# Optimization experiments

Measured on AMD Instinct MI355X. Metric: run time of the kernel, lower is better.

Reference implementation:

```python
import jax, jax.numpy as jnp
import numpy as np

D = 1024
H = 16
HD = D // H
FF = 4 * D
LN_EPS = 1e-5


def _layernorm(x, w, b):
    mu = jnp.mean(x, axis=-1, keepdims=True)
    var = jnp.mean(jnp.square(x - mu), axis=-1, keepdims=True)
    return (x - mu) * jax.lax.rsqrt(var + LN_EPS) * w + b


def setup_inputs() -> dict:
    key = jax.random.key(0)
    ks = jax.random.split(key, 12)
    s = 0.02
    return {
        "x": jax.random.normal(ks[0], (8, 1024, D), jnp.float32),
        "c": jax.random.normal(ks[1], (8, D), jnp.float32),
        "ln1_w": jnp.ones((D,), jnp.float32),
        "ln1_b": jnp.zeros((D,), jnp.float32),
        "ln2_w": jnp.ones((D,), jnp.float32),
        "ln2_b": jnp.zeros((D,), jnp.float32),
        "ada_w": jax.random.normal(ks[2], (D, 6 * D), jnp.float32) * s,
        "ada_b": jnp.zeros((6 * D,), jnp.float32),
        "qkv_w": jax.random.normal(ks[3], (D, 3 * D), jnp.float32) * s,
        "qkv_b": jnp.zeros((3 * D,), jnp.float32),
        "proj_w": jax.random.normal(ks[4], (D, D), jnp.float32) * s,
        "proj_b": jnp.zeros((D,), jnp.float32),
        "fc1_w": jax.random.normal(ks[5], (D, FF), jnp.float32) * s,
        "fc1_b": jnp.zeros((FF,), jnp.float32),
        "fc2_w": jax.random.normal(ks[6], (FF, D), jnp.float32) * s,
        "fc2_b": jnp.zeros((D,), jnp.float32),
    }


def reference(x, c, ln1_w, ln1_b, ln2_w, ln2_b, ada_w, ada_b,
              qkv_w, qkv_b, proj_w, proj_b, fc1_w, fc1_b, fc2_w, fc2_b):
    B, L, _ = x.shape
    # adaLN modulation: SiLU(c) @ W -> 6 chunks of (B, D)
    ssg = jax.nn.silu(c) @ ada_w + ada_b
    msa_shift, msa_scale, msa_gate, mlp_shift, mlp_scale, mlp_gate = jnp.split(ssg, 6, axis=-1)

    def modulate(h, shift, scale):
        return h * (1.0 + scale[:, None, :]) + shift[:, None, :]

    # ---- attention branch ----
    h = modulate(_layernorm(x, ln1_w, ln1_b), msa_shift, msa_scale)
    qkv = h @ qkv_w + qkv_b                      # (B, L, 3D)
    q, k, v = jnp.split(qkv, 3, axis=-1)
    q = q.reshape(B, L, H, HD).transpose(0, 2, 1, 3)   # (B, H, L, HD)
    k = k.reshape(B, L, H, HD).transpose(0, 2, 1, 3)
    v = v.reshape(B, L, H, HD).transpose(0, 2, 1, 3)
    scores = jnp.einsum("bhqd,bhkd->bhqk", q, k) / jnp.sqrt(jnp.float32(HD))
    attn = jax.nn.softmax(scores, axis=-1)
    a = jnp.einsum("bhqk,bhkd->bhqd", attn, v)   # (B, H, L, HD)
    a = a.transpose(0, 2, 1, 3).reshape(B, L, D)
    a = a @ proj_w + proj_b
    x = x + msa_gate[:, None, :] * a

    # ---- MLP branch ----
    h = modulate(_layernorm(x, ln2_w, ln2_b), mlp_shift, mlp_scale)
    h = jax.nn.gelu(h @ fc1_w + fc1_b, approximate=True)
    h = h @ fc2_w + fc2_b
    x = x + mlp_gate[:, None, :] * h
    return x
```

## Files before the change

### kernel.cpp

```cpp
#include <hip/hip_runtime.h>
#include <math.h>

#define DMODEL 1024
#define SIXD   6144
#define NHEAD  16
#define HEADD  64
#define LSEQ   1024
#define NBATCH 8
#define MROWS  8192

typedef unsigned short ushort_t;
typedef __attribute__((ext_vector_type(8))) short bf16x8;
typedef __attribute__((ext_vector_type(4))) float f32x4;

__device__ __forceinline__ unsigned short f2bf(float f) {
  unsigned int u = __float_as_uint(f);
  u += 0x7fff + ((u >> 16) & 1);
  return (unsigned short)(u >> 16);
}

__device__ __forceinline__ void gload_lds16(const void* g, void* l) {
  __builtin_amdgcn_global_load_lds(
      (const __attribute__((address_space(1))) unsigned int*)g,
      (__attribute__((address_space(3))) unsigned int*)l, 16, 0, 0);
}

__global__ void tcast_kernel(const float* __restrict__ W, ushort_t* __restrict__ WT,
                             int K, int N) {
  __shared__ float tile[32][33];
  int tx = threadIdx.x & 31, ty = threadIdx.x >> 5;
  int n0 = blockIdx.x * 32, k0 = blockIdx.y * 32;
#pragma unroll
  for (int r = 0; r < 4; ++r)
    tile[ty + 8*r][tx] = W[(size_t)(k0 + ty + 8*r) * N + n0 + tx];
  __syncthreads();
#pragma unroll
  for (int r = 0; r < 4; ++r)
    WT[(size_t)(n0 + ty + 8*r) * K + k0 + tx] = f2bf(tile[tx][ty + 8*r]);
}

__global__ __launch_bounds__(256) void vtrans_kernel(
    const ushort_t* __restrict__ qkvb, ushort_t* __restrict__ vT) {
  __shared__ ushort_t tile[128][66];
  int bh = blockIdx.x;
  int kt = blockIdx.y;
  int b = bh >> 4, h = bh & 15;
  int tid = threadIdx.x;
#pragma unroll
  for (int i = 0; i < 4; ++i) {
    int flat = tid + 256 * i;
    int r = flat >> 3, c8 = flat & 7;
    bf16x8 v = *(const bf16x8*)((const short*)qkvb +
        (size_t)(b * LSEQ + kt * 128 + r) * 3072 + 2048 + h * 64 + c8 * 8);
#pragma unroll
    for (int j = 0; j < 8; ++j) tile[r][c8 * 8 + j] = (ushort_t)v[j];
  }
  __syncthreads();
#pragma unroll
  for (int i = 0; i < 4; ++i) {
    int d = i * 16 + (tid >> 4);
    int kc = tid & 15;
    bf16x8 ov;
#pragma unroll
    for (int j = 0; j < 8; ++j) ov[j] = (short)tile[kc * 8 + j][d];
    *(bf16x8*)((short*)vT + (size_t)(bh * 64 + d) * 1024 + kt * 128 + kc * 8) = ov;
  }
}

__global__ void ada_kernel(const float* __restrict__ c, const float* __restrict__ ada_w,
                           const float* __restrict__ ada_b, float* __restrict__ ssg) {
  __shared__ float s[DMODEL];
  int b = blockIdx.y;
  int j = blockIdx.x * 256 + threadIdx.x;
  for (int i = threadIdx.x; i < DMODEL; i += 256) {
    float v = c[b * DMODEL + i];
    s[i] = v / (1.0f + __expf(-v));
  }
  __syncthreads();
  float acc = ada_b[j];
#pragma unroll 8
  for (int k = 0; k < DMODEL; ++k)
    acc = fmaf(s[k], ada_w[(size_t)k * SIXD + j], acc);
  ssg[b * SIXD + j] = acc;
}

__global__ __launch_bounds__(256) void ln_mod_kernel(
    const float* __restrict__ xin, const float* __restrict__ lw,
    const float* __restrict__ lb, const float* __restrict__ ssg,
    int shift_off, int scale_off, ushort_t* __restrict__ outB) {
  int row = blockIdx.x;
  int b = row >> 10;
  int tid = threadIdx.x;
  float4 v = ((const float4*)xin)[(size_t)row * 256 + tid];
  float sum = v.x + v.y + v.z + v.w;
  float sq  = v.x*v.x + v.y*v.y + v.z*v.z + v.w*v.w;
#pragma unroll
  for (int m = 32; m; m >>= 1) { sum += __shfl_xor(sum, m); sq += __shfl_xor(sq, m); }
  __shared__ float rbuf[8];
  int w = tid >> 6, lane = tid & 63;
  if (lane == 0) { rbuf[w] = sum; rbuf[4 + w] = sq; }
  __syncthreads();
  sum = rbuf[0] + rbuf[1] + rbuf[2] + rbuf[3];
  sq  = rbuf[4] + rbuf[5] + rbuf[6] + rbuf[7];
  float mu  = sum * (1.0f / 1024.0f);
  float var = sq * (1.0f / 1024.0f) - mu * mu;
  float rs  = rsqrtf(var + 1e-5f);
  const float* sg = ssg + b * SIXD;
  float vv[4] = {v.x, v.y, v.z, v.w};
  ushort4 pk;
  unsigned short* pks = (unsigned short*)&pk;
#pragma unroll
  for (int j = 0; j < 4; ++j) {
    int d = tid * 4 + j;
    float h = (vv[j] - mu) * rs * lw[d] + lb[d];
    h = h * (1.0f + sg[scale_off + d]) + sg[shift_off + d];
    pks[j] = f2bf(h);
  }
  ((ushort4*)outB)[(size_t)row * 256 + tid] = pk;
}

template <int EPI>
__global__ __launch_bounds__(256, 2) void gemm_kernel(
    const ushort_t* __restrict__ A, const ushort_t* __restrict__ BT,
    const float* __restrict__ bias, const float* __restrict__ ssg,
    const float* resid, float* outF, ushort_t* __restrict__ outB,
    int N, int K, int gate_off) {
  __shared__ __align__(16) char As[16384];
  __shared__ __align__(16) char Bs[16384];
  int tid = threadIdx.x, lane = tid & 63, w = tid >> 6;
  int l15 = lane & 15, g = lane >> 4;
  int m0 = blockIdx.y * 128, n0 = blockIdx.x * 128;
  int wrow = (w >> 1) * 64, wcol = (w & 1) * 64;
  f32x4 zero = {0.f, 0.f, 0.f, 0.f};
  f32x4 acc[4][4];
#pragma unroll
  for (int i = 0; i < 4; ++i)
#pragma unroll
    for (int j = 0; j < 4; ++j) acc[i][j] = zero;

  for (int k0 = 0; k0 < K; k0 += 64) {
#pragma unroll
    for (int p = 0; p < 4; ++p) {
      int flat = p * 4096 + w * 1024 + lane * 16;
      int row = flat >> 7;
      int colb = (flat & 127) ^ ((row & 7) << 4);
      gload_lds16((const char*)A  + ((size_t)(m0 + row) * K + k0) * 2 + colb,
                  As + p * 4096 + w * 1024);
      gload_lds16((const char*)BT + ((size_t)(n0 + row) * K + k0) * 2 + colb,
                  Bs + p * 4096 + w * 1024);
    }
    __syncthreads();
#pragma unroll
    for (int kk = 0; kk < 2; ++kk) {
      bf16x8 af[4], bfr[4];
#pragma unroll
      for (int i = 0; i < 4; ++i) {
        int ar = wrow + i * 16 + l15;
        af[i]  = *(const bf16x8*)(As + ar * 128 + ((kk * 64 + g * 16) ^ ((ar & 7) << 4)));
        int br = wcol + i * 16 + l15;
        bfr[i] = *(const bf16x8*)(Bs + br * 128 + ((kk * 64 + g * 16) ^ ((br & 7) << 4)));
      }
#pragma unroll
      for (int i = 0; i < 4; ++i)
#pragma unroll
        for (int j = 0; j < 4; ++j)
          acc[i][j] = __builtin_amdgcn_mfma_f32_16x16x32_bf16(af[i], bfr[j], acc[i][j], 0, 0, 0);
    }
    __syncthreads();
  }
#pragma unroll
  for (int i = 0; i < 4; ++i)
#pragma unroll
    for (int j = 0; j < 4; ++j)
#pragma unroll
      for (int r = 0; r < 4; ++r) {
        int grow = m0 + wrow + i * 16 + g * 4 + r;
        int gcol = n0 + wcol + j * 16 + l15;
        float v = acc[i][j][r] + bias[gcol];
        if (EPI == 0) {
          outB[(size_t)grow * N + gcol] = f2bf(v);
        } else if (EPI == 1 || EPI == 3) {
          int bb = grow >> 10;
          float gate = ssg[bb * SIXD + gate_off + gcol];
          size_t idx = (size_t)grow * N + gcol;
          outF[idx] = resid[idx] + gate * v;
        } else {
          float u = v;
          float t = 0.7978845608028654f * (u + 0.044715f * u * u * u);
          float e = __expf(2.0f * t);
          float th = 1.0f - 2.0f / (e + 1.0f);
          outB[(size_t)grow * N + gcol] = f2bf(0.5f * u * (1.0f + th));
        }
      }
}

__global__ __launch_bounds__(256, 2) void attn_kernel(
    const ushort_t* __restrict__ qkv,
    const ushort_t* __restrict__ vT,
    ushort_t* __restrict__ aout) {
  __shared__ __align__(16) char SM[33024];
  float* alphab = (float*)(SM + 32768);
  int tid = threadIdx.x, lane = tid & 63, w = tid >> 6;
  int l15 = lane & 15, g = lane >> 4;
  int qt = blockIdx.x, bh = blockIdx.y;
  int b = bh >> 4, h = bh & 15;

  bf16x8 aq[2];
  {
    int qrow = qt * 64 + w * 16 + l15;
    const short* qp = (const short*)qkv + (size_t)(b * LSEQ + qrow) * 3072 + h * 64 + g * 8;
    aq[0] = *(const bf16x8*)qp;
    aq[1] = *(const bf16x8*)(qp + 32);
  }

  const char* ksrc[2];
  const char* vsrc[2];
#pragma unroll
  for (int p = 0; p < 2; ++p) {
    int flat = p * 4096 + w * 1024 + lane * 16;
    int row = flat >> 7;
    int colb = (flat & 127) ^ ((row & 7) << 4);
    ksrc[p] = (const char*)qkv + ((size_t)(b * LSEQ + row) * 3072 + 1024 + h * 64) * 2 + colb;
    vsrc[p] = (const char*)vT + ((size_t)(bh * 64 + row) * 1024) * 2 + colb;
  }

  f32x4 zero = {0.f, 0.f, 0.f, 0.f};
  f32x4 o[4] = {zero, zero, zero, zero};
  float mrow = -INFINITY;
  float lrow = 0.f;
  const float sc = 0.18033688f;

#pragma unroll
  for (int p = 0; p < 2; ++p) {
    gload_lds16(ksrc[p], SM + p * 4096 + w * 1024);
    gload_lds16(vsrc[p], SM + 16384 + p * 4096 + w * 1024);
  }
  __syncthreads();

  for (int t = 0; t < 16; ++t) {
    int cur = t & 1;
    if (t < 15) {
      size_t koff = (size_t)(t + 1) * (64 * 3072 * 2);
      size_t voff = (size_t)(t + 1) * 128;
#pragma unroll
      for (int p = 0; p < 2; ++p) {
        gload_lds16(ksrc[p] + koff, SM + (cur ^ 1) * 8192 + p * 4096 + w * 1024);
        gload_lds16(vsrc[p] + voff, SM + 16384 + (cur ^ 1) * 8192 + p * 4096 + w * 1024);
      }
    }
    f32x4 s4[4] = {zero, zero, zero, zero};
#pragma unroll
    for (int c = 0; c < 4; ++c)
#pragma unroll
      for (int ks = 0; ks < 2; ++ks) {
        int key = c * 16 + l15;
        bf16x8 ak = *(const bf16x8*)(SM + cur * 8192 + key * 128 +
                                     ((ks * 64 + g * 16) ^ ((key & 7) << 4)));
        s4[c] = __builtin_amdgcn_mfma_f32_16x16x32_bf16(ak, aq[ks], s4[c], 0, 0, 0);
      }
    float z[16], mx = -INFINITY;
#pragma unroll
    for (int c = 0; c < 4; ++c)
#pragma unroll
      for (int r = 0; r < 4; ++r) {
        float t2 = s4[c][r] * sc;
        z[c * 4 + r] = t2;
        mx = fmaxf(mx, t2);
      }
    mx = fmaxf(mx, __shfl_xor(mx, 16));
    mx = fmaxf(mx, __shfl_xor(mx, 32));
    bool need = __any(mx > mrow);
    if (need) {
      float mnew = fmaxf(mrow, mx);
      float alpha = exp2f(mrow - mnew);
      mrow = mnew;
      if (lane < 16) alphab[w * 16 + lane] = alpha;
      lrow *= alpha;
    }
    float p16[16], sump = 0.f;
#pragma unroll
    for (int i = 0; i < 16; ++i) {
      float p = exp2f(z[i] - mrow);
      p16[i] = p;
      sump += p;
    }
    sump += __shfl_xor(sump, 16);
    sump += __shfl_xor(sump, 32);
    lrow += sump;
    if (need) {
      f32x4 av = *(const f32x4*)&alphab[w * 16 + g * 4];
#pragma unroll
      for (int nb = 0; nb < 4; ++nb)
#pragma unroll
        for (int r = 0; r < 4; ++r) o[nb][r] *= av[r];
    }
    unsigned pk[8];
#pragma unroll
    for (int c = 0; c < 4; ++c)
#pragma unroll
      for (int m = 0; m < 2; ++m)
        asm("v_cvt_pk_bf16_f32 %0, %1, %2"
            : "=v"(pk[c * 2 + m]) : "v"(p16[c * 4 + 2 * m]), "v"(p16[c * 4 + 2 * m + 1]));
    unsigned pa[2][4];
    int gl = (g & 1) * 2;
#pragma unroll
    for (int kb = 0; kb < 2; ++kb)
#pragma unroll
      for (int wv = 0; wv < 4; ++wv) {
        int srcl = l15 + (gl + (wv >> 1)) * 16;
        unsigned vA = (unsigned)__shfl((int)pk[kb * 4 + (wv & 1)], srcl);
        unsigned vB = (unsigned)__shfl((int)pk[kb * 4 + 2 + (wv & 1)], srcl);
        pa[kb][wv] = (g >> 1) ? vB : vA;
      }
    union PU { unsigned u[4]; bf16x8 v; };
    PU pu0, pu1;
#pragma unroll
    for (int i = 0; i < 4; ++i) { pu0.u[i] = pa[0][i]; pu1.u[i] = pa[1][i]; }
#pragma unroll
    for (int kb = 0; kb < 2; ++kb)
#pragma unroll
      for (int nb = 0; nb < 4; ++nb) {
        int d = nb * 16 + l15;
        bf16x8 bv = *(const bf16x8*)(SM + 16384 + cur * 8192 + d * 128 +
                                     ((kb * 64 + g * 16) ^ ((d & 7) << 4)));
        o[nb] = __builtin_amdgcn_mfma_f32_16x16x32_bf16(kb ? pu1.v : pu0.v, bv, o[nb], 0, 0, 0);
      }
    __syncthreads();
  }
  if (lane < 16) alphab[w * 16 + lane] = 1.0f / lrow;
  f32x4 rl = *(const f32x4*)&alphab[w * 16 + g * 4];
#pragma unroll
  for (int nb = 0; nb < 4; ++nb)
#pragma unroll
    for (int r = 0; r < 4; ++r) {
      int qrow = qt * 64 + w * 16 + g * 4 + r;
      aout[(size_t)(b * LSEQ + qrow) * 1024 + h * 64 + nb * 16 + l15] =
          f2bf(o[nb][r] * rl[r]);
    }
}

extern "C" void kernel_launch(void* const* d_in, const int* in_sizes, int n_in,
                              void* d_out, int out_size, void* d_ws, size_t ws_size,
                              hipStream_t stream) {
  const float* x      = (const float*)d_in[0];
  const float* c      = (const float*)d_in[1];
  const float* ln1_w  = (const float*)d_in[2];
  const float* ln1_b  = (const float*)d_in[3];
  const float* ln2_w  = (const float*)d_in[4];
  const float* ln2_b  = (const float*)d_in[5];
  const float* ada_w  = (const float*)d_in[6];
  const float* ada_b  = (const float*)d_in[7];
  const float* qkv_w  = (const float*)d_in[8];
  const float* qkv_b  = (const float*)d_in[9];
  const float* proj_w = (const float*)d_in[10];
  const float* proj_b = (const float*)d_in[11];
  const float* fc1_w  = (const float*)d_in[12];
  const float* fc1_b  = (const float*)d_in[13];
  const float* fc2_w  = (const float*)d_in[14];
  const float* fc2_b  = (const float*)d_in[15];
  float* out = (float*)d_out;
  char* ws = (char*)d_ws;

  ushort_t* qkvT  = (ushort_t*)(ws + 0);
  ushort_t* projT = (ushort_t*)(ws + 6291456);
  ushort_t* fc1T  = (ushort_t*)(ws + 8388608);
  ushort_t* fc2T  = (ushort_t*)(ws + 16777216);
  float*    ssg   = (float*)(ws + 25165824);
  ushort_t* hbuf  = (ushort_t*)(ws + 25362432);
  ushort_t* abuf  = hbuf;
  ushort_t* qkvb  = (ushort_t*)(ws + 42139648);
  ushort_t* vTb   = (ushort_t*)(ws + 92471296);
  if (ws_size < (size_t)109248512) return;

  tcast_kernel<<<dim3(96, 32),  256, 0, stream>>>(qkv_w,  qkvT, 1024, 3072);
  tcast_kernel<<<dim3(32, 32),  256, 0, stream>>>(proj_w, projT, 1024, 1024);
  tcast_kernel<<<dim3(128, 32), 256, 0, stream>>>(fc1_w,  fc1T, 1024, 4096);
  tcast_kernel<<<dim3(32, 128), 256, 0, stream>>>(fc2_w,  fc2T, 4096, 1024);
  ada_kernel<<<dim3(24, 8), 256, 0, stream>>>(c, ada_w, ada_b, ssg);

  ln_mod_kernel<<<8192, 256, 0, stream>>>(x, ln1_w, ln1_b, ssg, 0, 1024, hbuf);
  gemm_kernel<0><<<dim3(24, 64), 256, 0, stream>>>(hbuf, qkvT, qkv_b, nullptr,
                                                   nullptr, nullptr, qkvb, 3072, 1024, 0);
  vtrans_kernel<<<dim3(128, 8), 256, 0, stream>>>(qkvb, vTb);
  attn_kernel<<<dim3(16, 128), 256, 0, stream>>>(qkvb, vTb, abuf);
  gemm_kernel<1><<<dim3(8, 64), 256, 0, stream>>>(abuf, projT, proj_b, ssg,
                                                  x, out, nullptr, 1024, 1024, 2048);
  ln_mod_kernel<<<8192, 256, 0, stream>>>(out, ln2_w, ln2_b, ssg, 3072, 4096, hbuf);
  gemm_kernel<2><<<dim3(32, 64), 256, 0, stream>>>(hbuf, fc1T, fc1_b, nullptr,
                                                   nullptr, nullptr, qkvb, 4096, 1024, 0);
  gemm_kernel<3><<<dim3(8, 64), 256, 0, stream>>>(qkvb, fc2T, fc2_b, ssg,
                                                  out, out, nullptr, 1024, 4096, 5120);
}
```

Measured before the change: 443.2 us.

## Restructure GEMM into 256x128 tiles with triple-buffered LDS pipeline and XCD swizzle

Rewrites the bf16 MFMA GEMM to use 512-thread blocks with 256x128 output tiles and a three-stage global-to-LDS pipeline using direct LDS loads. Explicit vmcnt waits and raw barriers overlap loads with compute, and s_setprio raises priority during the MFMA section. Block indices are remapped so neighbouring tiles land on the same XCD for L2 reuse. This trades 144KB of LDS per block, allowing only one block per CU, for less load latency exposure and better operand reuse.

```diff
diff --git a/kernel.cpp b/kernel.cpp
--- a/kernel.cpp
+++ b/kernel.cpp
@@ -120,74 +120,113 @@
 }
 
 template <int EPI>
-__global__ __launch_bounds__(256, 2) void gemm_kernel(
+__global__ __launch_bounds__(512, 2) void gemm_kernel(
     const ushort_t* __restrict__ A, const ushort_t* __restrict__ BT,
     const float* __restrict__ bias, const float* __restrict__ ssg,
     const float* resid, float* outF, ushort_t* __restrict__ outB,
-    int N, int K, int gate_off) {
-  __shared__ __align__(16) char As[16384];
-  __shared__ __align__(16) char Bs[16384];
-  int tid = threadIdx.x, lane = tid & 63, w = tid >> 6;
+    int N, int K, int gate_off, int ntx) {
+  __shared__ __align__(16) char SM[147456];
+  int tid = threadIdx.x, lane = tid & 63;
   int l15 = lane & 15, g = lane >> 4;
-  int m0 = blockIdx.y * 128, n0 = blockIdx.x * 128;
-  int wrow = (w >> 1) * 64, wcol = (w & 1) * 64;
+  int w = tid >> 6, wm = w >> 2, wn = w & 3;
+  int nwg = gridDim.x, orig = blockIdx.x;
+  int wg = (orig & 7) * (nwg >> 3) + (orig >> 3);
+  int bx = wg % ntx, by = wg / ntx;
+  int m0 = by * 256, n0 = bx * 128;
+
+  const char* asrc[4];
+  const char* bsrc[2];
+#pragma unroll
+  for (int ch = 0; ch < 4; ++ch) {
+    int flat = ch * 8192 + tid * 16;
+    int row = flat >> 7;
+    int colb = (flat & 127) ^ ((row & 7) << 4);
+    asrc[ch] = (const char*)A + ((size_t)(m0 + row) * K) * 2 + colb;
+  }
+#pragma unroll
+  for (int ch = 0; ch < 2; ++ch) {
+    int flat = ch * 8192 + tid * 16;
+    int row = flat >> 7;
+    int colb = (flat & 127) ^ ((row & 7) << 4);
+    bsrc[ch] = (const char*)BT + ((size_t)(n0 + row) * K) * 2 + colb;
+  }
+
   f32x4 zero = {0.f, 0.f, 0.f, 0.f};
-  f32x4 acc[4][4];
-#pragma unroll
-  for (int i = 0; i < 4; ++i)
-#pragma unroll
-    for (int j = 0; j < 4; ++j) acc[i][j] = zero;
-
-  for (int k0 = 0; k0 < K; k0 += 64) {
-#pragma unroll
-    for (int p = 0; p < 4; ++p) {
-      int flat = p * 4096 + w * 1024 + lane * 16;
-      int row = flat >> 7;
-      int colb = (flat & 127) ^ ((row & 7) << 4);
-      gload_lds16((const char*)A  + ((size_t)(m0 + row) * K + k0) * 2 + colb,
-                  As + p * 4096 + w * 1024);
-      gload_lds16((const char*)BT + ((size_t)(n0 + row) * K + k0) * 2 + colb,
-                  Bs + p * 4096 + w * 1024);
-    }
-    __syncthreads();
+  f32x4 acc[8][2];
+#pragma unroll
+  for (int i = 0; i < 8; ++i) { acc[i][0] = zero; acc[i][1] = zero; }
+
+  auto STAGE = [&](int t, int s) {
+    char* base = SM + s * 49152;
+    size_t ko = (size_t)t * 128;
+#pragma unroll
+    for (int ch = 0; ch < 4; ++ch)
+      gload_lds16(asrc[ch] + ko, base + ch * 8192 + tid * 16);
+#pragma unroll
+    for (int ch = 0; ch < 2; ++ch)
+      gload_lds16(bsrc[ch] + ko, base + 32768 + ch * 8192 + tid * 16);
+  };
+
+  int T = K >> 6;
+  STAGE(0, 0);
+  STAGE(1, 1);
+  int s0 = 0;
+  for (int t = 0; t < T; ++t) {
+    int s2 = s0 + 2; if (s2 >= 3) s2 -= 3;
+    if (t + 2 < T) STAGE(t + 2, s2);
+    int rem = T - 1 - t;
+    if (rem >= 2)      asm volatile("s_waitcnt vmcnt(12)" ::: "memory");
+    else if (rem == 1) asm volatile("s_waitcnt vmcnt(6)" ::: "memory");
+    else               asm volatile("s_waitcnt vmcnt(0)" ::: "memory");
+    asm volatile("s_barrier" ::: "memory");
+    const char* ab = SM + s0 * 49152;
+    const char* bb = ab + 32768;
+    bf16x8 af[2][8], bfr[2][2];
 #pragma unroll
     for (int kk = 0; kk < 2; ++kk) {
-      bf16x8 af[4], bfr[4];
-#pragma unroll
-      for (int i = 0; i < 4; ++i) {
-        int ar = wrow + i * 16 + l15;
-        af[i]  = *(const bf16x8*)(As + ar * 128 + ((kk * 64 + g * 16) ^ ((ar & 7) << 4)));
-        int br = wcol + i * 16 + l15;
-        bfr[i] = *(const bf16x8*)(Bs + br * 128 + ((kk * 64 + g * 16) ^ ((br & 7) << 4)));
-      }
-#pragma unroll
-      for (int i = 0; i < 4; ++i)
-#pragma unroll
-        for (int j = 0; j < 4; ++j)
-          acc[i][j] = __builtin_amdgcn_mfma_f32_16x16x32_bf16(af[i], bfr[j], acc[i][j], 0, 0, 0);
-    }
-    __syncthreads();
-  }
-#pragma unroll
-  for (int i = 0; i < 4; ++i)
-#pragma unroll
-    for (int j = 0; j < 4; ++j)
+#pragma unroll
+      for (int i = 0; i < 8; ++i) {
+        int ar = wm * 128 + i * 16 + l15;
+        af[kk][i] = *(const bf16x8*)(ab + ar * 128 + ((kk * 64 + g * 16) ^ ((ar & 7) << 4)));
+      }
+#pragma unroll
+      for (int j = 0; j < 2; ++j) {
+        int br = wn * 32 + j * 16 + l15;
+        bfr[kk][j] = *(const bf16x8*)(bb + br * 128 + ((kk * 64 + g * 16) ^ ((br & 7) << 4)));
+      }
+    }
+    __builtin_amdgcn_s_setprio(1);
+#pragma unroll
+    for (int kk = 0; kk < 2; ++kk)
+#pragma unroll
+      for (int i = 0; i < 8; ++i)
+#pragma unroll
+        for (int j = 0; j < 2; ++j)
+          acc[i][j] = __builtin_amdgcn_mfma_f32_16x16x32_bf16(af[kk][i], bfr[kk][j], acc[i][j], 0, 0, 0);
+    __builtin_amdgcn_s_setprio(0);
+    asm volatile("s_barrier" ::: "memory");
+    s0 = s0 + 1; if (s0 >= 3) s0 -= 3;
+  }
+#pragma unroll
+  for (int i = 0; i < 8; ++i)
+#pragma unroll
+    for (int j = 0; j < 2; ++j)
 #pragma unroll
       for (int r = 0; r < 4; ++r) {
-        int grow = m0 + wrow + i * 16 + g * 4 + r;
-        int gcol = n0 + wcol + j * 16 + l15;
+        int grow = m0 + wm * 128 + i * 16 + g * 4 + r;
+        int gcol = n0 + wn * 32 + j * 16 + l15;
         float v = acc[i][j][r] + bias[gcol];
         if (EPI == 0) {
           outB[(size_t)grow * N + gcol] = f2bf(v);
         } else if (EPI == 1 || EPI == 3) {
-          int bb = grow >> 10;
-          float gate = ssg[bb * SIXD + gate_off + gcol];
+          int bb2 = grow >> 10;
+          float gate = ssg[bb2 * SIXD + gate_off + gcol];
           size_t idx = (size_t)grow * N + gcol;
           outF[idx] = resid[idx] + gate * v;
         } else {
           float u = v;
-          float t = 0.7978845608028654f * (u + 0.044715f * u * u * u);
-          float e = __expf(2.0f * t);
+          float tt = 0.7978845608028654f * (u + 0.044715f * u * u * u);
+          float e = __expf(2.0f * tt);
           float th = 1.0f - 2.0f / (e + 1.0f);
           outB[(size_t)grow * N + gcol] = f2bf(0.5f * u * (1.0f + th));
         }
@@ -379,15 +418,15 @@
   ada_kernel<<<dim3(24, 8), 256, 0, stream>>>(c, ada_w, ada_b, ssg);
 
   ln_mod_kernel<<<8192, 256, 0, stream>>>(x, ln1_w, ln1_b, ssg, 0, 1024, hbuf);
-  gemm_kernel<0><<<dim3(24, 64), 256, 0, stream>>>(hbuf, qkvT, qkv_b, nullptr,
-                                                   nullptr, nullptr, qkvb, 3072, 1024, 0);
+  gemm_kernel<0><<<768, 512, 0, stream>>>(hbuf, qkvT, qkv_b, nullptr,
+                                          nullptr, nullptr, qkvb, 3072, 1024, 0, 24);
   vtrans_kernel<<<dim3(128, 8), 256, 0, stream>>>(qkvb, vTb);
   attn_kernel<<<dim3(16, 128), 256, 0, stream>>>(qkvb, vTb, abuf);
-  gemm_kernel<1><<<dim3(8, 64), 256, 0, stream>>>(abuf, projT, proj_b, ssg,
-                                                  x, out, nullptr, 1024, 1024, 2048);
+  gemm_kernel<1><<<256, 512, 0, stream>>>(abuf, projT, proj_b, ssg,
+                                          x, out, nullptr, 1024, 1024, 2048, 8);
   ln_mod_kernel<<<8192, 256, 0, stream>>>(out, ln2_w, ln2_b, ssg, 3072, 4096, hbuf);
-  gemm_kernel<2><<<dim3(32, 64), 256, 0, stream>>>(hbuf, fc1T, fc1_b, nullptr,
-                                                   nullptr, nullptr, qkvb, 4096, 1024, 0);
-  gemm_kernel<3><<<dim3(8, 64), 256, 0, stream>>>(qkvb, fc2T, fc2_b, ssg,
-                                                  out, out, nullptr, 1024, 4096, 5120);
-}
+  gemm_kernel<2><<<1024, 512, 0, stream>>>(hbuf, fc1T, fc1_b, nullptr,
+                                           nullptr, nullptr, qkvb, 4096, 1024, 0, 32);
+  gemm_kernel<3><<<256, 512, 0, stream>>>(qkvb, fc2T, fc2_b, ssg,
+                                          out, out, nullptr, 1024, 4096, 5120, 8);
+}
```

New measurement: 467.3 us. 5.4% more time.

## Double-buffer GEMM LDS tiles to overlap global loads with MFMA compute

Applied to the files above, without the earlier changes.

The GEMM kernel now uses a 64KB shared buffer split into two stages. It issues the async global-to-LDS loads for the next K tile before computing on the current one, and waits with an explicit vmcnt(8) count plus a raw s_barrier instead of __syncthreads. This is meant to hide global memory latency behind the MFMA work in all four projection GEMMs. In exchange, LDS use per block doubles, which pressures the two-blocks-per-CU occupancy target, and correctness now rests on hand-written wait counts.

```diff
diff --git a/kernel.cpp b/kernel.cpp
--- a/kernel.cpp
+++ b/kernel.cpp
@@ -125,8 +125,7 @@
     const float* __restrict__ bias, const float* __restrict__ ssg,
     const float* resid, float* outF, ushort_t* __restrict__ outB,
     int N, int K, int gate_off) {
-  __shared__ __align__(16) char As[16384];
-  __shared__ __align__(16) char Bs[16384];
+  __shared__ __align__(16) char SM[65536];
   int tid = threadIdx.x, lane = tid & 63, w = tid >> 6;
   int l15 = lane & 15, g = lane >> 4;
   int m0 = blockIdx.y * 128, n0 = blockIdx.x * 128;
@@ -138,27 +137,51 @@
 #pragma unroll
     for (int j = 0; j < 4; ++j) acc[i][j] = zero;
 
-  for (int k0 = 0; k0 < K; k0 += 64) {
-#pragma unroll
-    for (int p = 0; p < 4; ++p) {
-      int flat = p * 4096 + w * 1024 + lane * 16;
-      int row = flat >> 7;
-      int colb = (flat & 127) ^ ((row & 7) << 4);
-      gload_lds16((const char*)A  + ((size_t)(m0 + row) * K + k0) * 2 + colb,
-                  As + p * 4096 + w * 1024);
-      gload_lds16((const char*)BT + ((size_t)(n0 + row) * K + k0) * 2 + colb,
-                  Bs + p * 4096 + w * 1024);
-    }
-    __syncthreads();
+  const char* asrc[4];
+  const char* bsrc[4];
+#pragma unroll
+  for (int ch = 0; ch < 4; ++ch) {
+    int flat = ch * 4096 + tid * 16;
+    int row = flat >> 7;
+    int colb = (flat & 127) ^ ((row & 7) << 4);
+    asrc[ch] = (const char*)A  + ((size_t)(m0 + row) * K) * 2 + colb;
+    bsrc[ch] = (const char*)BT + ((size_t)(n0 + row) * K) * 2 + colb;
+  }
+
+  int T = K >> 6;
+#pragma unroll
+  for (int ch = 0; ch < 4; ++ch)
+    gload_lds16(asrc[ch], SM + ch * 4096 + tid * 16);
+#pragma unroll
+  for (int ch = 0; ch < 4; ++ch)
+    gload_lds16(bsrc[ch], SM + 16384 + ch * 4096 + tid * 16);
+
+  for (int t = 0; t < T; ++t) {
+    if (t + 1 < T) {
+      char* base = SM + ((t + 1) & 1) * 32768;
+      size_t ko = (size_t)(t + 1) * 128;
+#pragma unroll
+      for (int ch = 0; ch < 4; ++ch)
+        gload_lds16(asrc[ch] + ko, base + ch * 4096 + tid * 16);
+#pragma unroll
+      for (int ch = 0; ch < 4; ++ch)
+        gload_lds16(bsrc[ch] + ko, base + 16384 + ch * 4096 + tid * 16);
+      asm volatile("s_waitcnt vmcnt(8)" ::: "memory");
+    } else {
+      asm volatile("s_waitcnt vmcnt(0)" ::: "memory");
+    }
+    asm volatile("s_barrier" ::: "memory");
+    const char* ab = SM + (t & 1) * 32768;
+    const char* bb = ab + 16384;
 #pragma unroll
     for (int kk = 0; kk < 2; ++kk) {
       bf16x8 af[4], bfr[4];
 #pragma unroll
       for (int i = 0; i < 4; ++i) {
         int ar = wrow + i * 16 + l15;
-        af[i]  = *(const bf16x8*)(As + ar * 128 + ((kk * 64 + g * 16) ^ ((ar & 7) << 4)));
+        af[i]  = *(const bf16x8*)(ab + ar * 128 + ((kk * 64 + g * 16) ^ ((ar & 7) << 4)));
         int br = wcol + i * 16 + l15;
-        bfr[i] = *(const bf16x8*)(Bs + br * 128 + ((kk * 64 + g * 16) ^ ((br & 7) << 4)));
+        bfr[i] = *(const bf16x8*)(bb + br * 128 + ((kk * 64 + g * 16) ^ ((br & 7) << 4)));
       }
 #pragma unroll
       for (int i = 0; i < 4; ++i)
@@ -166,7 +189,7 @@
         for (int j = 0; j < 4; ++j)
           acc[i][j] = __builtin_amdgcn_mfma_f32_16x16x32_bf16(af[i], bfr[j], acc[i][j], 0, 0, 0);
     }
-    __syncthreads();
+    asm volatile("s_barrier" ::: "memory");
   }
 #pragma unroll
   for (int i = 0; i < 4; ++i)
@@ -180,14 +203,14 @@
         if (EPI == 0) {
           outB[(size_t)grow * N + gcol] = f2bf(v);
         } else if (EPI == 1 || EPI == 3) {
-          int bb = grow >> 10;
-          float gate = ssg[bb * SIXD + gate_off + gcol];
+          int bb2 = grow >> 10;
+          float gate = ssg[bb2 * SIXD + gate_off + gcol];
           size_t idx = (size_t)grow * N + gcol;
           outF[idx] = resid[idx] + gate * v;
         } else {
           float u = v;
-          float t = 0.7978845608028654f * (u + 0.044715f * u * u * u);
-          float e = __expf(2.0f * t);
+          float t2 = 0.7978845608028654f * (u + 0.044715f * u * u * u);
+          float e = __expf(2.0f * t2);
           float th = 1.0f - 2.0f / (e + 1.0f);
           outB[(size_t)grow * N + gcol] = f2bf(0.5f * u * (1.0f + th));
         }
```

Measured after the change: 460.5 us. 3.9% more time.
